# Performance work log

Measured on AMD Instinct MI355X. Metric: run time of the kernel, lower is better.

The kernel has to match this reference:

```python
import jax, jax.numpy as jnp
import numpy as np

E = 768      # embed_dim
H = 12       # num_heads
D = E // H   # head_dim = 64
G = 8        # num_groups (grouped 1x1 conv)
MAX_S = 197  # max_seq_len
RED = 8      # SE reduction ratio
S, B = 197, 64


def grouped_linear(x, w, b):
    """Grouped 1x1 conv as grouped linear. x: [..., Cin], w: [Cout, Cin//G], b: [Cout]."""
    cout = w.shape[0]
    cin = x.shape[-1]
    xg = x.reshape(x.shape[:-1] + (G, cin // G))
    wg = w.reshape(G, cout // G, cin // G)
    y = jnp.einsum('...gi,goi->...go', xg, wg)
    return y.reshape(x.shape[:-1] + (cout,)) + b


def channel_shuffle(x):
    """Shuffle channels (last dim) across G groups, matching torch channel_shuffle."""
    c = x.shape[-1]
    xg = x.reshape(x.shape[:-1] + (G, c // G))
    return jnp.swapaxes(xg, -1, -2).reshape(x.shape)


def layernorm(x, g, b, eps=1e-5):
    mu = jnp.mean(x, axis=-1, keepdims=True)
    var = jnp.var(x, axis=-1, keepdims=True)
    return (x - mu) * jax.lax.rsqrt(var + eps) * g + b


def setup_inputs() -> dict:
    rng = jax.random.key(0)
    ks = jax.random.split(rng, 16)
    std = 0.02
    return {
        'query': jax.random.normal(ks[0], (S, B, E), jnp.float32),
        'key':   jax.random.normal(ks[1], (S, B, E), jnp.float32),
        'value': jax.random.normal(ks[2], (S, B, E), jnp.float32),
        'qkv_w': jax.random.normal(ks[3], (3 * E, E // G), jnp.float32) * std,
        'qkv_b': jnp.zeros((3 * E,), jnp.float32),
        'out_w': jax.random.normal(ks[4], (E, E // G), jnp.float32) * std,
        'out_b': jnp.zeros((E,), jnp.float32),
        'rel_pos': jax.random.normal(ks[5], (2 * MAX_S - 1, D), jnp.float32) * std,
        'ln_g': jnp.ones((E,), jnp.float32),
        'ln_b': jnp.zeros((E,), jnp.float32),
        'fc1_w': jax.random.normal(ks[6], (E, E // RED), jnp.float32) * std,
        'fc1_b': jnp.zeros((E // RED,), jnp.float32),
        'fc2_w': jax.random.normal(ks[7], (E // RED, E), jnp.float32) * std,
        'fc2_b': jnp.zeros((E,), jnp.float32),
    }


def reference(query, key, value, qkv_w, qkv_b, out_w, out_b, rel_pos,
              ln_g, ln_b, fc1_w, fc1_b, fc2_w, fc2_b):
    seq_len, bsz, embed_dim = query.shape
    scaling = float(D) ** -0.5

    x = jnp.transpose(query, (1, 0, 2))              # [B, S, E]
    qkv = grouped_linear(x, qkv_w, qkv_b)            # [B, S, 3E]
    qkv = channel_shuffle(qkv)                       # [B, S, 3E]
    q, k, v = jnp.split(qkv, 3, axis=-1)             # each [B, S, E]

    def heads(t):                                    # [B, S, E] -> [B, H, S, D]
        return jnp.transpose(t.reshape(bsz, seq_len, H, D), (0, 2, 1, 3))
    q, k, v = heads(q) * scaling, heads(k), heads(v)

    attn_w = jnp.einsum('bhsd,bhtd->bhst', q, k)     # content-content

    # decoupled relative-position attention (note: slice, not skew, per source)
    rel = rel_pos[MAX_S - seq_len: MAX_S + seq_len - 1]           # [2S-1, D]
    content_pos = jnp.einsum('bhsd,rd->bhsr', q, rel)[..., seq_len - 1: 2 * seq_len - 1]
    pos_content = jnp.einsum('rd,bhtd->bhrt', rel, k)[:, :, seq_len - 1: 2 * seq_len - 1, :]
    attn_w = attn_w + content_pos + pos_content

    probs = jax.nn.softmax(attn_w, axis=-1)          # [B, H, S, S]
    attn = jnp.einsum('bhst,bhtd->bhsd', probs, v)   # [B, H, S, D]
    attn = jnp.transpose(attn, (0, 2, 1, 3)).reshape(bsz, seq_len, E)  # [B, S, E]

    # squeeze-excite style feature calibration gating
    scale = jax.nn.sigmoid(
        jnp.dot(jax.nn.gelu(jnp.dot(layernorm(attn, ln_g, ln_b), fc1_w) + fc1_b), fc2_w) + fc2_b)
    attn = attn * scale

    out = grouped_linear(attn, out_w, out_b)         # [B, S, E]
    out = jnp.transpose(out, (1, 0, 2))              # [S, B, E]

    avg_weights = jnp.sum(probs, axis=1) / H         # [B, S, S]
    return out, avg_weights
```

## Files before the change

### kernel.cpp

```cpp
#include <hip/hip_runtime.h>
#include <hip/hip_bf16.h>

constexpr int S = 197;
constexpr int B = 64;
constexpr int E = 768;
constexpr int H = 12;
constexpr int D = 64;
constexpr int M = S * B;
constexpr size_t SBE = (size_t)M * E;
constexpr int PST = 208;

typedef short bf16x8 __attribute__((ext_vector_type(8)));
typedef float f32x4 __attribute__((ext_vector_type(4)));
typedef unsigned int u32x4 __attribute__((ext_vector_type(4)));

__device__ __forceinline__ unsigned short f2b(float x) {
  unsigned int u = __float_as_uint(x);
  return (unsigned short)((u + 0x7FFFu + ((u >> 16) & 1u)) >> 16);
}
__device__ __forceinline__ float b2f(unsigned short u) {
  return __uint_as_float((unsigned int)u << 16);
}

__global__ __launch_bounds__(256) void mha_wprep(const float* __restrict__ w1,
                                                 const float* __restrict__ w2,
                                                 const float* __restrict__ lng,
                                                 const float* __restrict__ lnb,
                                                 const float* __restrict__ b1,
                                                 const float* __restrict__ rel,
                                                 const float* __restrict__ wq,
                                                 unsigned short* __restrict__ w1t,
                                                 unsigned short* __restrict__ w2t,
                                                 float* __restrict__ cgb,
                                                 float* __restrict__ cbb,
                                                 unsigned short* __restrict__ relb,
                                                 unsigned short* __restrict__ wqt) {
  const int bid = blockIdx.x, tid = threadIdx.x;
  if (bid < 288) {
    int idx = bid * 256 + tid;
    int n = idx / 768, k = idx - n * 768;
    w1t[idx] = f2b(lng[k] * w1[(size_t)k * 96 + n]);
  } else if (bid < 576) {
    int idx = (bid - 288) * 256 + tid;
    int n = idx / 96, k = idx - n * 96;
    w2t[idx] = f2b(w2[(size_t)k * 768 + n]);
  } else if (bid == 576) {
    if (tid < 96) {
      float cg = 0.f, cb = 0.f;
      for (int k = 0; k < 768; ++k) {
        float wv = w1[(size_t)k * 96 + tid];
        cg += lng[k] * wv;
        cb += lnb[k] * wv;
      }
      cgb[tid] = cg;
      cbb[tid] = cb + b1[tid];
    }
  } else if (bid < 641) {
    int idx = (bid - 577) * 256 + tid;
    int s2 = idx >> 6, d = idx & 63;
    float v = (s2 < S) ? rel[(size_t)(S - 1 + s2) * D + d] : 0.f;
    relb[idx] = f2b(v);
  } else {
    int idx = (bid - 641) * 256 + tid;
    wqt[idx] = f2b(wq[idx]);
  }
}

__global__ __launch_bounds__(256) void mha_qkv_gemm(const float* __restrict__ x,
                                                    const unsigned short* __restrict__ wqt,
                                                    const float* __restrict__ bias,
                                                    unsigned short* __restrict__ y) {
  __shared__ __align__(16) unsigned short Wl[288 * 104];
  __shared__ float bias_s[288];
  const int m0 = blockIdx.x * 64;
  const int g = blockIdx.y;
  const int tid = threadIdx.x;
  const int lane = tid & 63, wv = tid >> 6;
  const int l15 = lane & 15, l4 = lane >> 4;

  for (int i = tid; i < 288 * 12; i += 256) {
    int n = i / 12, c8 = i - n * 12;
    *(u32x4*)(Wl + n * 104 + c8 * 8) =
        *(const u32x4*)(wqt + (size_t)(g * 288 + n) * 96 + c8 * 8);
  }
  for (int i = tid; i < 288; i += 256) bias_s[i] = bias[g * 288 + i];

  const float* xr = x + (size_t)(m0 + 16 * wv + l15) * E + g * 96 + l4 * 8;
  auto ldfrag = [](const float* p) -> bf16x8 {
    float4 u = *reinterpret_cast<const float4*>(p);
    float4 v = *reinterpret_cast<const float4*>(p + 4);
    unsigned short t[8] = {f2b(u.x), f2b(u.y), f2b(u.z), f2b(u.w),
                           f2b(v.x), f2b(v.y), f2b(v.z), f2b(v.w)};
    return *(const bf16x8*)t;
  };
  bf16x8 a0 = ldfrag(xr);
  bf16x8 a1 = ldfrag(xr + 32);
  bf16x8 a2 = ldfrag(xr + 64);
  __syncthreads();

  const int mloc = m0 + 16 * wv + 4 * l4;
#pragma unroll
  for (int nf = 0; nf < 18; ++nf) {
    const unsigned short* wr = Wl + (nf * 16 + l15) * 104 + l4 * 8;
    f32x4 a = (f32x4){0.f, 0.f, 0.f, 0.f};
    a = __builtin_amdgcn_mfma_f32_16x16x32_bf16(a0, *(const bf16x8*)(wr), a, 0, 0, 0);
    a = __builtin_amdgcn_mfma_f32_16x16x32_bf16(a1, *(const bf16x8*)(wr + 32), a, 0, 0, 0);
    a = __builtin_amdgcn_mfma_f32_16x16x32_bf16(a2, *(const bf16x8*)(wr + 64), a, 0, 0, 0);
    int ploc = nf * 16 + l15;
    int p = g * 288 + ploc;
    float bv = bias_s[ploc];
#pragma unroll
    for (int r = 0; r < 4; ++r)
      y[(size_t)(mloc + r) * 2304 + p] = f2b(a[r] + bv);
  }
}

__global__ __launch_bounds__(256) void mha_qkv_shuffle(const unsigned short* __restrict__ y,
                                                       const float* __restrict__ rel,
                                                       unsigned short* __restrict__ qb,
                                                       unsigned short* __restrict__ kb,
                                                       unsigned short* __restrict__ vb) {
  const int tid = threadIdx.x;
  const int lane = tid & 63;
  const int g = lane >> 3, j = lane & 7;
  const int d = j * 8 + g;
  const int wrow = tid >> 6;
  const int rbase = blockIdx.x * 16;

  float relv[4];
  int sA[4], bA[4];
#pragma unroll
  for (int r8 = 0; r8 < 4; ++r8) {
    int rowl = rbase + r8 * 4 + wrow;
    sA[r8] = rowl >> 6;
    bA[r8] = rowl & 63;
    relv[r8] = rel[(size_t)(S - 1 + sA[r8]) * D + d];
  }

  for (int h = 0; h < H; ++h) {
#pragma unroll
    for (int r8 = 0; r8 < 4; ++r8) {
      int rowl = rbase + r8 * 4 + wrow;
      const unsigned short* yr = y + (size_t)rowl * 2304 + g * 288 + h * 8 + j;
      size_t o = (((size_t)bA[r8] * H + h) * S + sA[r8]) * D + d;
      float vq = b2f(yr[0]);
      float vk = b2f(yr[96]);
      float vv = b2f(yr[192]);
      qb[o] = f2b(0.125f * vq + relv[r8]);
      kb[o] = f2b(vk + relv[r8]);
      vb[o] = f2b(vv);
    }
  }
}

__global__ __launch_bounds__(512) void mha_fattn(
    const unsigned short* __restrict__ qb, const unsigned short* __restrict__ kb,
    const unsigned short* __restrict__ vb, const unsigned short* __restrict__ relb,
    unsigned short* __restrict__ ctxb, unsigned short* __restrict__ probs, int bh0) {
  __shared__ __align__(16) unsigned short KtPt[128 * 136];
  __shared__ __align__(16) unsigned short Vh[64 * 136];
  unsigned short* Kt = KtPt;
  unsigned short* Pt = KtPt;

  const int id = blockIdx.x;
  const int xcd = id & 7;
  const int rr = id >> 3;
  const int stile = rr & 1;
  const int bhl = xcd + 8 * (rr >> 1);
  const int bh = bh0 + bhl;
  const int b_ = bh / H, h_ = bh - b_ * H;
  const int s0 = stile * 128;
  const int tid = threadIdx.x;
  const int lane = tid & 63, w = tid >> 6;
  const int l15 = lane & 15, l4 = lane >> 4;
  const int vt = tid & 63;
  const int vdb = (tid >> 6) * 8;

  const unsigned short* qg = qb + (((size_t)bh * S + (s0 + 16 * w + l15)) << 6) + l4 * 8;
  const unsigned short* rg = relb + (((size_t)((s0 + 16 * w + l15) & 255)) << 6) + l4 * 8;
  bf16x8 aq0 = *(const bf16x8*)(qg);
  bf16x8 aq1 = *(const bf16x8*)(qg + 32);
  bf16x8 aq2 = *(const bf16x8*)(rg);
  bf16x8 aq3 = *(const bf16x8*)(rg + 32);

  const int kr = tid >> 3, kc = tid & 7;
  auto loadK = [&](int tc, u32x4& kv, u32x4& rv) {
    int tg = tc * 64 + kr;
    kv = (u32x4){0, 0, 0, 0};
    rv = (u32x4){0, 0, 0, 0};
    if (tg < S) {
      kv = *(const u32x4*)(kb + (((size_t)bh * S + tg) << 6) + kc * 8);
      u32x4 rvv = *(const u32x4*)(relb + ((size_t)tg << 6) + kc * 8);
      rv = rvv ^ 0x80008000u;
    }
  };

  f32x4 acc[13];
#pragma unroll
  for (int i = 0; i < 13; ++i) acc[i] = (f32x4){0.f, 0.f, 0.f, 0.f};

  u32x4 kvA, rvA, kvB, rvB;
  loadK(0, kvA, rvA);
  *(u32x4*)(Kt + kr * 136 + kc * 8) = kvA;
  *(u32x4*)(Kt + kr * 136 + 64 + kc * 8) = rvA;
  loadK(1, kvB, rvB);
  __syncthreads();

#pragma unroll
  for (int tc = 0; tc < 4; ++tc) {
    const int boff = (tc & 1) * 64 * 136;
    if (tc < 3) {
      u32x4 skv = (tc & 1) ? kvA : kvB;
      u32x4 srv = (tc & 1) ? rvA : rvB;
      const int sboff = ((tc + 1) & 1) * 64 * 136;
      *(u32x4*)(Kt + sboff + kr * 136 + kc * 8) = skv;
      *(u32x4*)(Kt + sboff + kr * 136 + 64 + kc * 8) = srv;
      if (tc == 0) loadK(2, kvA, rvA);
      else if (tc == 1) loadK(3, kvB, rvB);
    }
#pragma unroll
    for (int tf = 0; tf < 4; ++tf) {
      if (tc == 3 && tf > 0) continue;
      const unsigned short* kbse = Kt + boff + (tf * 16 + l15) * 136 + l4 * 8;
      f32x4 a = acc[tc * 4 + tf];
      a = __builtin_amdgcn_mfma_f32_16x16x32_bf16(aq0, *(const bf16x8*)(kbse), a, 0, 0, 0);
      a = __builtin_amdgcn_mfma_f32_16x16x32_bf16(aq1, *(const bf16x8*)(kbse + 32), a, 0, 0, 0);
      a = __builtin_amdgcn_mfma_f32_16x16x32_bf16(aq2, *(const bf16x8*)(kbse + 64), a, 0, 0, 0);
      a = __builtin_amdgcn_mfma_f32_16x16x32_bf16(aq3, *(const bf16x8*)(kbse + 96), a, 0, 0, 0);
      acc[tc * 4 + tf] = a;
    }
    __syncthreads();
  }

  u32x4 v1[2];
#pragma unroll
  for (int ii = 0; ii < 2; ++ii) {
    int t = ii * 64 + vt;
    v1[ii] = *(const u32x4*)(vb + (((size_t)bh * S + t) << 6) + vdb);
  }

  if (l15 >= 5) acc[12] = (f32x4){-3.0e38f, -3.0e38f, -3.0e38f, -3.0e38f};
  float inv[4];
#pragma unroll
  for (int r = 0; r < 4; ++r) {
    float m = acc[0][r];
#pragma unroll
    for (int tf = 1; tf < 13; ++tf) m = fmaxf(m, acc[tf][r]);
#pragma unroll
    for (int off = 1; off < 16; off <<= 1) m = fmaxf(m, __shfl_xor(m, off, 64));
    float s = 0.f;
#pragma unroll
    for (int tf = 0; tf < 13; ++tf) {
      float e = __expf(acc[tf][r] - m);
      acc[tf][r] = e;
      s += e;
    }
#pragma unroll
    for (int off = 1; off < 16; off <<= 1) s += __shfl_xor(s, off, 64);
    inv[r] = 1.f / s;
  }

  f32x4 ov[4];
#pragma unroll
  for (int df = 0; df < 4; ++df) ov[df] = (f32x4){0.f, 0.f, 0.f, 0.f};

#pragma unroll
  for (int tf = 0; tf < 8; ++tf)
#pragma unroll
    for (int r = 0; r < 4; ++r)
      Pt[(16 * w + 4 * l4 + r) * 136 + tf * 16 + l15] = f2b(acc[tf][r] * inv[r]);
#pragma unroll
  for (int ii = 0; ii < 2; ++ii) {
    int t = ii * 64 + vt;
    const unsigned short* vp = (const unsigned short*)&v1[ii];
#pragma unroll
    for (int j = 0; j < 8; ++j) Vh[(vdb + j) * 136 + t] = vp[j];
  }
  __syncthreads();

  u32x4 v2[2];
#pragma unroll
  for (int ii = 0; ii < 2; ++ii) {
    int t = 128 + ii * 64 + vt;
    v2[ii] = (u32x4){0, 0, 0, 0};
    if (t < S) v2[ii] = *(const u32x4*)(vb + (((size_t)bh * S + t) << 6) + vdb);
  }

  {
    const int r2 = tid >> 2;
    const int sg = s0 + r2;
    if (sg < S) {
#pragma unroll
      for (int j = 0; j < 4; ++j) {
        int c = (tid & 3) + 4 * j;
        u32x4 pv = *(const u32x4*)(Pt + r2 * 136 + c * 8);
        *(u32x4*)(probs + ((size_t)bhl * S + sg) * PST + c * 8) = pv;
      }
    }
  }
  {
    bf16x8 ap[4];
#pragma unroll
    for (int kf = 0; kf < 4; ++kf)
      ap[kf] = *(const bf16x8*)(Pt + (16 * w + l15) * 136 + kf * 32 + l4 * 8);
#pragma unroll
    for (int df = 0; df < 4; ++df) {
      const unsigned short* vbse = Vh + (df * 16 + l15) * 136 + l4 * 8;
      f32x4 o = ov[df];
#pragma unroll
      for (int kf = 0; kf < 4; ++kf)
        o = __builtin_amdgcn_mfma_f32_16x16x32_bf16(ap[kf], *(const bf16x8*)(vbse + kf * 32), o, 0, 0, 0);
      ov[df] = o;
    }
  }
  __syncthreads();

#pragma unroll
  for (int tf = 8; tf < 13; ++tf)
#pragma unroll
    for (int r = 0; r < 4; ++r)
      Pt[(16 * w + 4 * l4 + r) * 136 + (tf - 8) * 16 + l15] = f2b(acc[tf][r] * inv[r]);
#pragma unroll
  for (int r = 0; r < 4; ++r)
    Pt[(16 * w + 4 * l4 + r) * 136 + 80 + l15] = 0;
#pragma unroll
  for (int ii = 0; ii < 2; ++ii) {
    int t0h = ii * 64 + vt;
    if (t0h < 96) {
      const unsigned short* vp = (const unsigned short*)&v2[ii];
#pragma unroll
      for (int j = 0; j < 8; ++j) Vh[(vdb + j) * 136 + t0h] = vp[j];
    }
  }
  __syncthreads();

  {
    const int r2 = tid >> 2;
    const int sg = s0 + r2;
    if (sg < S) {
#pragma unroll
      for (int j = 0; j < 3; ++j) {
        int c = (tid & 3) + 4 * j;
        if (c < 10) {
          u32x4 pv = *(const u32x4*)(Pt + r2 * 136 + c * 8);
          *(u32x4*)(probs + ((size_t)bhl * S + sg) * PST + 128 + c * 8) = pv;
        }
      }
    }
  }
  {
    bf16x8 ap[3];
#pragma unroll
    for (int kf = 0; kf < 3; ++kf)
      ap[kf] = *(const bf16x8*)(Pt + (16 * w + l15) * 136 + kf * 32 + l4 * 8);
#pragma unroll
    for (int df = 0; df < 4; ++df) {
      const unsigned short* vbse = Vh + (df * 16 + l15) * 136 + l4 * 8;
      f32x4 o = ov[df];
#pragma unroll
      for (int kf = 0; kf < 3; ++kf)
        o = __builtin_amdgcn_mfma_f32_16x16x32_bf16(ap[kf], *(const bf16x8*)(vbse + kf * 32), o, 0, 0, 0);
      ov[df] = o;
    }
  }

#pragma unroll
  for (int df = 0; df < 4; ++df)
#pragma unroll
    for (int r = 0; r < 4; ++r) {
      int sg = s0 + 16 * w + 4 * l4 + r;
      if (sg < S)
        ctxb[((size_t)b_ * S + sg) * E + h_ * 64 + df * 16 + l15] = f2b(ov[df][r]);
    }
}

__global__ __launch_bounds__(256) void mha_avgred(const unsigned short* __restrict__ probs,
                                                  float* __restrict__ avg, int b0) {
  const int bs = blockIdx.x;
  const int bl = bs / S, s = bs - bl * S;
  const int t = threadIdx.x;
  if (t >= S) return;
  float acc = 0.f;
#pragma unroll
  for (int h = 0; h < H; ++h)
    acc += b2f(probs[(((size_t)bl * H + h) * S + s) * PST + t]);
  avg[(((size_t)(b0 + bl)) * S + s) * S + t] = acc * (1.f / H);
}

__global__ __launch_bounds__(128) void mha_fc1ln(const unsigned short* __restrict__ ctxb,
                                                 const unsigned short* __restrict__ w1t,
                                                 const float* __restrict__ cgb,
                                                 const float* __restrict__ cbb,
                                                 unsigned short* __restrict__ h1) {
  __shared__ __align__(16) unsigned short As[32 * 104];
  __shared__ __align__(16) unsigned short Wl[48 * 104];
  __shared__ float smu[32], sinv[32];
  const int m0 = blockIdx.x * 32;
  const int n0 = blockIdx.y * 48;
  const int tid = threadIdx.x;
  const int lane = tid & 63, w = tid >> 6;
  const int l15 = lane & 15, l4 = lane >> 4;
  const int r = tid >> 2, q = tid & 3;

  float s1 = 0.f, s2 = 0.f;
  f32x4 acc[3];
#pragma unroll
  for (int nf = 0; nf < 3; ++nf) acc[nf] = (f32x4){0.f, 0.f, 0.f, 0.f};

  for (int c = 0; c < 8; ++c) {
    const int k0 = c * 96;
    {
      const unsigned short* xr = ctxb + (size_t)(m0 + r) * E + k0 + q * 24;
      unsigned short loc[24];
      *(u32x4*)(loc) = *(const u32x4*)(xr);
      *(u32x4*)(loc + 8) = *(const u32x4*)(xr + 8);
      *(u32x4*)(loc + 16) = *(const u32x4*)(xr + 16);
      unsigned short* ar = As + r * 104 + q * 24;
      *(u32x4*)(ar) = *(const u32x4*)(loc);
      *(u32x4*)(ar + 8) = *(const u32x4*)(loc + 8);
      *(u32x4*)(ar + 16) = *(const u32x4*)(loc + 16);
#pragma unroll
      for (int j = 0; j < 24; ++j) {
        float v = b2f(loc[j]);
        s1 += v;
        s2 += v * v;
      }
    }
    for (int i = tid; i < 48 * 12; i += 128) {
      int n = i / 12, c8 = i - n * 12;
      *(u32x4*)(Wl + n * 104 + c8 * 8) =
          *(const u32x4*)(w1t + (size_t)(n0 + n) * E + k0 + c8 * 8);
    }
    __syncthreads();
    const unsigned short* arow = As + (16 * w + l15) * 104 + l4 * 8;
    bf16x8 a0 = *(const bf16x8*)(arow);
    bf16x8 a1 = *(const bf16x8*)(arow + 32);
    bf16x8 a2 = *(const bf16x8*)(arow + 64);
#pragma unroll
    for (int nf = 0; nf < 3; ++nf) {
      const unsigned short* wr = Wl + (nf * 16 + l15) * 104 + l4 * 8;
      f32x4 a = acc[nf];
      a = __builtin_amdgcn_mfma_f32_16x16x32_bf16(a0, *(const bf16x8*)(wr), a, 0, 0, 0);
      a = __builtin_amdgcn_mfma_f32_16x16x32_bf16(a1, *(const bf16x8*)(wr + 32), a, 0, 0, 0);
      a = __builtin_amdgcn_mfma_f32_16x16x32_bf16(a2, *(const bf16x8*)(wr + 64), a, 0, 0, 0);
      acc[nf] = a;
    }
    __syncthreads();
  }

  s1 += __shfl_xor(s1, 1, 64); s1 += __shfl_xor(s1, 2, 64);
  s2 += __shfl_xor(s2, 1, 64); s2 += __shfl_xor(s2, 2, 64);
  if (q == 0) {
    float mu = s1 * (1.f / E);
    float var = s2 * (1.f / E) - mu * mu;
    smu[r] = mu;
    sinv[r] = rsqrtf(var + 1e-5f);
  }
  __syncthreads();

#pragma unroll
  for (int nf = 0; nf < 3; ++nf) {
    int n = n0 + nf * 16 + l15;
    float cg = cgb[n], cb = cbb[n];
#pragma unroll
    for (int rr = 0; rr < 4; ++rr) {
      int ml = 16 * w + 4 * l4 + rr;
      float u = sinv[ml] * (acc[nf][rr] - smu[ml] * cg) + cb;
      float gl = 0.5f * u * (1.f + tanhf(0.7978845608028654f * (u + 0.044715f * u * u * u)));
      h1[(size_t)(m0 + ml) * 96 + n] = f2b(gl);
    }
  }
}

__global__ __launch_bounds__(256) void mha_fc2(const unsigned short* __restrict__ h1,
                                               const unsigned short* __restrict__ w2t,
                                               const float* __restrict__ bias,
                                               const unsigned short* __restrict__ ctxb,
                                               unsigned short* __restrict__ attn2) {
  __shared__ __align__(16) unsigned short Hs[64 * 104];
  __shared__ __align__(16) unsigned short Wl[192 * 104];
  const int m0 = blockIdx.x * 64;
  const int n0 = blockIdx.y * 192;
  const int tid = threadIdx.x;
  const int lane = tid & 63, w = tid >> 6;
  const int l15 = lane & 15, l4 = lane >> 4;

  for (int i = tid; i < 64 * 12; i += 256) {
    int rr = i / 12, c8 = i - rr * 12;
    *(u32x4*)(Hs + rr * 104 + c8 * 8) =
        *(const u32x4*)(h1 + (size_t)(m0 + rr) * 96 + c8 * 8);
  }
  for (int i = tid; i < 192 * 12; i += 256) {
    int n = i / 12, c8 = i - n * 12;
    *(u32x4*)(Wl + n * 104 + c8 * 8) =
        *(const u32x4*)(w2t + (size_t)(n0 + n) * 96 + c8 * 8);
  }
  __syncthreads();

  const unsigned short* arow = Hs + (16 * w + l15) * 104 + l4 * 8;
  bf16x8 a0 = *(const bf16x8*)(arow);
  bf16x8 a1 = *(const bf16x8*)(arow + 32);
  bf16x8 a2 = *(const bf16x8*)(arow + 64);

#pragma unroll
  for (int nf = 0; nf < 12; ++nf) {
    const unsigned short* wr = Wl + (nf * 16 + l15) * 104 + l4 * 8;
    f32x4 a = (f32x4){0.f, 0.f, 0.f, 0.f};
    a = __builtin_amdgcn_mfma_f32_16x16x32_bf16(a0, *(const bf16x8*)(wr), a, 0, 0, 0);
    a = __builtin_amdgcn_mfma_f32_16x16x32_bf16(a1, *(const bf16x8*)(wr + 32), a, 0, 0, 0);
    a = __builtin_amdgcn_mfma_f32_16x16x32_bf16(a2, *(const bf16x8*)(wr + 64), a, 0, 0, 0);
    int n = n0 + nf * 16 + l15;
    float bv = bias[n];
#pragma unroll
    for (int rr = 0; rr < 4; ++rr) {
      int m = m0 + 16 * w + 4 * l4 + rr;
      float val = a[rr] + bv;
      float sg = 1.f / (1.f + __expf(-val));
      float cv = b2f(ctxb[(size_t)m * E + n]);
      attn2[(size_t)m * E + n] = f2b(cv * sg);
    }
  }
}

__global__ __launch_bounds__(256) void mha_out(const unsigned short* __restrict__ attn2,
                                               const float* __restrict__ w,
                                               const float* __restrict__ bias,
                                               float* __restrict__ outp) {
  __shared__ __align__(16) unsigned short Asl[64 * 104];
  __shared__ __align__(16) unsigned short Wl[96 * 104];
  __shared__ float bias_s[96];
  const int m0 = blockIdx.x * 64;
  const int g = blockIdx.y;
  const int n0 = g * 96;
  const int tid = threadIdx.x;
  const int lane = tid & 63, w_ = tid >> 6;
  const int l15 = lane & 15, l4 = lane >> 4;

  for (int i = tid; i < 64 * 12; i += 256) {
    int rr = i / 12, c8 = i - rr * 12;
    *(u32x4*)(Asl + rr * 104 + c8 * 8) =
        *(const u32x4*)(attn2 + (size_t)(m0 + rr) * E + n0 + c8 * 8);
  }
  for (int i = tid; i < 96 * 24; i += 256) {
    int n = i / 24, c4 = i - n * 24;
    float4 v = *reinterpret_cast<const float4*>(&w[(size_t)(n0 + n) * 96 + c4 * 4]);
    unsigned short* dst = Wl + n * 104 + c4 * 4;
    dst[0] = f2b(v.x); dst[1] = f2b(v.y); dst[2] = f2b(v.z); dst[3] = f2b(v.w);
  }
  if (tid < 96) bias_s[tid] = bias[n0 + tid];
  __syncthreads();

  const unsigned short* arow = Asl + (16 * w_ + l15) * 104 + l4 * 8;
  bf16x8 a0 = *(const bf16x8*)(arow);
  bf16x8 a1 = *(const bf16x8*)(arow + 32);
  bf16x8 a2 = *(const bf16x8*)(arow + 64);

  int bb4[4], ss4[4];
#pragma unroll
  for (int rr = 0; rr < 4; ++rr) {
    int m = m0 + 16 * w_ + 4 * l4 + rr;
    bb4[rr] = m / S;
    ss4[rr] = m - bb4[rr] * S;
  }

#pragma unroll
  for (int nf = 0; nf < 6; ++nf) {
    const unsigned short* wr = Wl + (nf * 16 + l15) * 104 + l4 * 8;
    f32x4 a = (f32x4){0.f, 0.f, 0.f, 0.f};
    a = __builtin_amdgcn_mfma_f32_16x16x32_bf16(a0, *(const bf16x8*)(wr), a, 0, 0, 0);
    a = __builtin_amdgcn_mfma_f32_16x16x32_bf16(a1, *(const bf16x8*)(wr + 32), a, 0, 0, 0);
    a = __builtin_amdgcn_mfma_f32_16x16x32_bf16(a2, *(const bf16x8*)(wr + 64), a, 0, 0, 0);
    int p = n0 + nf * 16 + l15;
    float bv = bias_s[p - n0];
#pragma unroll
    for (int rr = 0; rr < 4; ++rr)
      outp[((size_t)ss4[rr] * B + bb4[rr]) * E + p] = a[rr] + bv;
  }
}

extern "C" void kernel_launch(void* const* d_in, const int* in_sizes, int n_in,
                              void* d_out, int out_size, void* d_ws, size_t ws_size,
                              hipStream_t stream) {
  const float* query = (const float*)d_in[0];
  const float* qkv_w = (const float*)d_in[3];
  const float* qkv_b = (const float*)d_in[4];
  const float* out_w = (const float*)d_in[5];
  const float* out_b = (const float*)d_in[6];
  const float* rel   = (const float*)d_in[7];
  const float* ln_g  = (const float*)d_in[8];
  const float* ln_b  = (const float*)d_in[9];
  const float* fc1_w = (const float*)d_in[10];
  const float* fc1_b = (const float*)d_in[11];
  const float* fc2_w = (const float*)d_in[12];
  const float* fc2_b = (const float*)d_in[13];

  float* ws = (float*)d_ws;
  unsigned short* qb   = (unsigned short*)ws;
  unsigned short* kbuf = qb + SBE;
  unsigned short* vbb  = kbuf + SBE;
  unsigned short* relb = vbb + SBE;
  size_t off = 3 * SBE / 2 + 8192;
  float* context = ws + off;
  unsigned short* ctxb = (unsigned short*)context;
  unsigned short* attn2b = (unsigned short*)(ws + off + SBE);
  unsigned short* ybuf = (unsigned short*)context;
  unsigned short* h1b = attn2b + SBE;
  unsigned short* w1t = h1b + (size_t)M * 96;
  unsigned short* w2t = w1t + 73728;
  unsigned short* wqt = w2t + 73728;
  float* cgb = (float*)(wqt + 221184);
  float* cbb = cgb + 96;
  unsigned short* probsb = (unsigned short*)(cbb + 96);
  float* outp = (float*)d_out;
  float* avgp = outp + SBE;

  size_t used_f = off + SBE + (SBE + (size_t)M * 96 + 368640) / 2 + 192;
  size_t avail_f = (ws_size / 4 > used_f) ? ws_size / 4 - used_f : 0;
  int Bc = 2;
  const int cand[6] = {64, 32, 16, 8, 4, 2};
  for (int i = 0; i < 6; ++i) {
    size_t need_f = ((size_t)cand[i] * H * S * PST + 1) / 2;
    if (need_f <= avail_f) { Bc = cand[i]; break; }
  }

  mha_wprep<<<1505, 256, 0, stream>>>(fc1_w, fc2_w, ln_g, ln_b, fc1_b, rel, qkv_w,
                                      w1t, w2t, cgb, cbb, relb, wqt);

  mha_qkv_gemm<<<dim3(M / 64, 8), 256, 0, stream>>>(query, wqt, qkv_b, ybuf);
  mha_qkv_shuffle<<<M / 16, 256, 0, stream>>>(ybuf, rel, qb, kbuf, vbb);

  for (int b0 = 0; b0 < B; b0 += Bc) {
    int bc = (B - b0 < Bc) ? (B - b0) : Bc;
    int nbh = bc * H;
    mha_fattn<<<2 * nbh, 512, 0, stream>>>(qb, kbuf, vbb, relb, ctxb, probsb,
                                           b0 * H);
    mha_avgred<<<bc * S, 256, 0, stream>>>(probsb, avgp, b0);
  }

  mha_fc1ln<<<dim3(M / 32, 2), 128, 0, stream>>>(ctxb, w1t, cgb, cbb, h1b);
  mha_fc2<<<dim3(M / 64, 4), 256, 0, stream>>>(h1b, w2t, fc2_b, ctxb, attn2b);
  mha_out<<<dim3(M / 64, 8), 256, 0, stream>>>(attn2b, out_w, out_b, outp);
}
```

Before: 227.4 us.

## Fuse SE fc2 gating with grouped output projection; vectorize head-average reduction

Merges the fc2+sigmoid gating kernel with the grouped output projection. Each block computes the 96 gated channels of its group, keeps them in shared memory and immediately runs the out-projection, so the attn2 intermediate never goes to global memory and one launch is dropped. Each block now also reloads the h1 tile per group, with 8 column blocks instead of 4. Separately, the head-average reduction reads two bf16 values per thread and writes float2, halving its thread count.

After: 227.4 us. About the same (-0.0%).

```diff
diff --git a/kernel.cpp b/kernel.cpp
--- a/kernel.cpp
+++ b/kernel.cpp
@@ -374,17 +374,27 @@
     }
 }
 
-__global__ __launch_bounds__(256) void mha_avgred(const unsigned short* __restrict__ probs,
+__global__ __launch_bounds__(128) void mha_avgred(const unsigned short* __restrict__ probs,
                                                   float* __restrict__ avg, int b0) {
   const int bs = blockIdx.x;
   const int bl = bs / S, s = bs - bl * S;
-  const int t = threadIdx.x;
-  if (t >= S) return;
-  float acc = 0.f;
-#pragma unroll
-  for (int h = 0; h < H; ++h)
-    acc += b2f(probs[(((size_t)bl * H + h) * S + s) * PST + t]);
-  avg[(((size_t)(b0 + bl)) * S + s) * S + t] = acc * (1.f / H);
+  const int t2 = threadIdx.x * 2;
+  if (t2 >= S) return;
+  float a0 = 0.f, a1 = 0.f;
+#pragma unroll
+  for (int h = 0; h < H; ++h) {
+    unsigned int pv = *(const unsigned int*)(probs +
+        (((size_t)bl * H + h) * S + s) * PST + t2);
+    a0 += b2f((unsigned short)(pv & 0xFFFF));
+    a1 += b2f((unsigned short)(pv >> 16));
+  }
+  float* dst = avg + (((size_t)(b0 + bl)) * S + s) * S + t2;
+  if (t2 + 1 < S) {
+    float2 o = {a0 * (1.f / H), a1 * (1.f / H)};
+    *reinterpret_cast<float2*>(dst) = o;
+  } else {
+    dst[0] = a0 * (1.f / H);
+  }
 }
 
 __global__ __launch_bounds__(128) void mha_fc1ln(const unsigned short* __restrict__ ctxb,
@@ -472,106 +482,102 @@
   }
 }
 
-__global__ __launch_bounds__(256) void mha_fc2(const unsigned short* __restrict__ h1,
-                                               const unsigned short* __restrict__ w2t,
-                                               const float* __restrict__ bias,
-                                               const unsigned short* __restrict__ ctxb,
-                                               unsigned short* __restrict__ attn2) {
-  __shared__ __align__(16) unsigned short Hs[64 * 104];
-  __shared__ __align__(16) unsigned short Wl[192 * 104];
+__global__ __launch_bounds__(256) void mha_fc2out(const unsigned short* __restrict__ h1,
+                                                  const unsigned short* __restrict__ w2t,
+                                                  const float* __restrict__ b2,
+                                                  const unsigned short* __restrict__ ctxb,
+                                                  const float* __restrict__ ow,
+                                                  const float* __restrict__ ob,
+                                                  float* __restrict__ outp) {
+  __shared__ __align__(16) unsigned short HsA2[64 * 104];
+  __shared__ __align__(16) unsigned short W2l[96 * 104];
+  __shared__ __align__(16) unsigned short Wol[96 * 104];
+  __shared__ float b2_s[96], bo_s[96];
   const int m0 = blockIdx.x * 64;
-  const int n0 = blockIdx.y * 192;
+  const int g = blockIdx.y;
+  const int n0 = g * 96;
   const int tid = threadIdx.x;
   const int lane = tid & 63, w = tid >> 6;
   const int l15 = lane & 15, l4 = lane >> 4;
 
   for (int i = tid; i < 64 * 12; i += 256) {
     int rr = i / 12, c8 = i - rr * 12;
-    *(u32x4*)(Hs + rr * 104 + c8 * 8) =
+    *(u32x4*)(HsA2 + rr * 104 + c8 * 8) =
         *(const u32x4*)(h1 + (size_t)(m0 + rr) * 96 + c8 * 8);
   }
-  for (int i = tid; i < 192 * 12; i += 256) {
+  for (int i = tid; i < 96 * 12; i += 256) {
     int n = i / 12, c8 = i - n * 12;
-    *(u32x4*)(Wl + n * 104 + c8 * 8) =
+    *(u32x4*)(W2l + n * 104 + c8 * 8) =
         *(const u32x4*)(w2t + (size_t)(n0 + n) * 96 + c8 * 8);
   }
-  __syncthreads();
-
-  const unsigned short* arow = Hs + (16 * w + l15) * 104 + l4 * 8;
-  bf16x8 a0 = *(const bf16x8*)(arow);
-  bf16x8 a1 = *(const bf16x8*)(arow + 32);
-  bf16x8 a2 = *(const bf16x8*)(arow + 64);
-
-#pragma unroll
-  for (int nf = 0; nf < 12; ++nf) {
-    const unsigned short* wr = Wl + (nf * 16 + l15) * 104 + l4 * 8;
+  for (int i = tid; i < 96 * 24; i += 256) {
+    int n = i / 24, c4 = i - n * 24;
+    float4 v = *reinterpret_cast<const float4*>(&ow[(size_t)(n0 + n) * 96 + c4 * 4]);
+    unsigned short* dst = Wol + n * 104 + c4 * 4;
+    dst[0] = f2b(v.x); dst[1] = f2b(v.y); dst[2] = f2b(v.z); dst[3] = f2b(v.w);
+  }
+  if (tid < 96) {
+    b2_s[tid] = b2[n0 + tid];
+    bo_s[tid] = ob[n0 + tid];
+  }
+  __syncthreads();
+
+  bf16x8 a0, a1, a2;
+  {
+    const unsigned short* arow = HsA2 + (16 * w + l15) * 104 + l4 * 8;
+    a0 = *(const bf16x8*)(arow);
+    a1 = *(const bf16x8*)(arow + 32);
+    a2 = *(const bf16x8*)(arow + 64);
+  }
+  f32x4 acc[6];
+#pragma unroll
+  for (int nf = 0; nf < 6; ++nf) {
+    const unsigned short* wr = W2l + (nf * 16 + l15) * 104 + l4 * 8;
     f32x4 a = (f32x4){0.f, 0.f, 0.f, 0.f};
     a = __builtin_amdgcn_mfma_f32_16x16x32_bf16(a0, *(const bf16x8*)(wr), a, 0, 0, 0);
     a = __builtin_amdgcn_mfma_f32_16x16x32_bf16(a1, *(const bf16x8*)(wr + 32), a, 0, 0, 0);
     a = __builtin_amdgcn_mfma_f32_16x16x32_bf16(a2, *(const bf16x8*)(wr + 64), a, 0, 0, 0);
-    int n = n0 + nf * 16 + l15;
-    float bv = bias[n];
+    acc[nf] = a;
+  }
+  __syncthreads();
+
+#pragma unroll
+  for (int nf = 0; nf < 6; ++nf) {
+    int n = nf * 16 + l15;
+    float bv = b2_s[n];
 #pragma unroll
     for (int rr = 0; rr < 4; ++rr) {
-      int m = m0 + 16 * w + 4 * l4 + rr;
-      float val = a[rr] + bv;
+      int ml = 16 * w + 4 * l4 + rr;
+      float val = acc[nf][rr] + bv;
       float sg = 1.f / (1.f + __expf(-val));
-      float cv = b2f(ctxb[(size_t)m * E + n]);
-      attn2[(size_t)m * E + n] = f2b(cv * sg);
-    }
-  }
-}
-
-__global__ __launch_bounds__(256) void mha_out(const unsigned short* __restrict__ attn2,
-                                               const float* __restrict__ w,
-                                               const float* __restrict__ bias,
-                                               float* __restrict__ outp) {
-  __shared__ __align__(16) unsigned short Asl[64 * 104];
-  __shared__ __align__(16) unsigned short Wl[96 * 104];
-  __shared__ float bias_s[96];
-  const int m0 = blockIdx.x * 64;
-  const int g = blockIdx.y;
-  const int n0 = g * 96;
-  const int tid = threadIdx.x;
-  const int lane = tid & 63, w_ = tid >> 6;
-  const int l15 = lane & 15, l4 = lane >> 4;
-
-  for (int i = tid; i < 64 * 12; i += 256) {
-    int rr = i / 12, c8 = i - rr * 12;
-    *(u32x4*)(Asl + rr * 104 + c8 * 8) =
-        *(const u32x4*)(attn2 + (size_t)(m0 + rr) * E + n0 + c8 * 8);
-  }
-  for (int i = tid; i < 96 * 24; i += 256) {
-    int n = i / 24, c4 = i - n * 24;
-    float4 v = *reinterpret_cast<const float4*>(&w[(size_t)(n0 + n) * 96 + c4 * 4]);
-    unsigned short* dst = Wl + n * 104 + c4 * 4;
-    dst[0] = f2b(v.x); dst[1] = f2b(v.y); dst[2] = f2b(v.z); dst[3] = f2b(v.w);
-  }
-  if (tid < 96) bias_s[tid] = bias[n0 + tid];
-  __syncthreads();
-
-  const unsigned short* arow = Asl + (16 * w_ + l15) * 104 + l4 * 8;
-  bf16x8 a0 = *(const bf16x8*)(arow);
-  bf16x8 a1 = *(const bf16x8*)(arow + 32);
-  bf16x8 a2 = *(const bf16x8*)(arow + 64);
-
+      float cv = b2f(ctxb[(size_t)(m0 + ml) * E + n0 + n]);
+      HsA2[ml * 104 + n] = f2b(cv * sg);
+    }
+  }
+  __syncthreads();
+
+  {
+    const unsigned short* arow = HsA2 + (16 * w + l15) * 104 + l4 * 8;
+    a0 = *(const bf16x8*)(arow);
+    a1 = *(const bf16x8*)(arow + 32);
+    a2 = *(const bf16x8*)(arow + 64);
+  }
   int bb4[4], ss4[4];
 #pragma unroll
   for (int rr = 0; rr < 4; ++rr) {
-    int m = m0 + 16 * w_ + 4 * l4 + rr;
+    int m = m0 + 16 * w + 4 * l4 + rr;
     bb4[rr] = m / S;
     ss4[rr] = m - bb4[rr] * S;
   }
-
 #pragma unroll
   for (int nf = 0; nf < 6; ++nf) {
-    const unsigned short* wr = Wl + (nf * 16 + l15) * 104 + l4 * 8;
+    const unsigned short* wr = Wol + (nf * 16 + l15) * 104 + l4 * 8;
     f32x4 a = (f32x4){0.f, 0.f, 0.f, 0.f};
     a = __builtin_amdgcn_mfma_f32_16x16x32_bf16(a0, *(const bf16x8*)(wr), a, 0, 0, 0);
     a = __builtin_amdgcn_mfma_f32_16x16x32_bf16(a1, *(const bf16x8*)(wr + 32), a, 0, 0, 0);
     a = __builtin_amdgcn_mfma_f32_16x16x32_bf16(a2, *(const bf16x8*)(wr + 64), a, 0, 0, 0);
     int p = n0 + nf * 16 + l15;
-    float bv = bias_s[p - n0];
+    float bv = bo_s[nf * 16 + l15];
 #pragma unroll
     for (int rr = 0; rr < 4; ++rr)
       outp[((size_t)ss4[rr] * B + bb4[rr]) * E + p] = a[rr] + bv;
@@ -634,10 +640,10 @@
     int nbh = bc * H;
     mha_fattn<<<2 * nbh, 512, 0, stream>>>(qb, kbuf, vbb, relb, ctxb, probsb,
                                            b0 * H);
-    mha_avgred<<<bc * S, 256, 0, stream>>>(probsb, avgp, b0);
+    mha_avgred<<<bc * S, 128, 0, stream>>>(probsb, avgp, b0);
   }
 
   mha_fc1ln<<<dim3(M / 32, 2), 128, 0, stream>>>(ctxb, w1t, cgb, cbb, h1b);
-  mha_fc2<<<dim3(M / 64, 4), 256, 0, stream>>>(h1b, w2t, fc2_b, ctxb, attn2b);
-  mha_out<<<dim3(M / 64, 8), 256, 0, stream>>>(attn2b, out_w, out_b, outp);
-}
+  mha_fc2out<<<dim3(M / 64, 8), 256, 0, stream>>>(h1b, w2t, fc2_b, ctxb, out_w,
+                                                  out_b, outp);
+}
```
